# Performance work log

Hardware: AMD Instinct MI355X
Metric: run time of the kernel (lower is better)

Reference implementation:

```python
import jax, jax.numpy as jnp
import numpy as np

C = 0.01          # Poincare ball curvature 1/100
SQRT_C = 0.1
EPS = 1e-15
BALL_EPS = 4e-3   # geoopt float32 projx boundary epsilon


def _norm(x):
    return jnp.linalg.norm(x, axis=-1, keepdims=True)


def expmap0(u):
    n = jnp.maximum(_norm(u), EPS)
    return jnp.tanh(SQRT_C * n) * u / (SQRT_C * n)


def logmap0(x):
    n = jnp.maximum(_norm(x), EPS)
    t = jnp.clip(SQRT_C * n, -1.0 + 1e-7, 1.0 - 1e-7)
    return jnp.arctanh(t) * x / (SQRT_C * n)


def projx(x):
    maxnorm = (1.0 - BALL_EPS) / SQRT_C
    n = jnp.maximum(_norm(x), EPS)
    return jnp.where(n > maxnorm, x / n * maxnorm, x)


def mobius_matvec(M, x):
    xn = jnp.maximum(_norm(x), EPS)
    mx = x @ M.T
    mxn = jnp.maximum(_norm(mx), EPS)
    t = jnp.clip(SQRT_C * xn, -1.0 + 1e-7, 1.0 - 1e-7)
    res = jnp.tanh(mxn / xn * jnp.arctanh(t)) * mx / (mxn * SQRT_C)
    return jnp.where(jnp.all(mx == 0, axis=-1, keepdims=True), 0.0, res)


def mobius_add(x, y):
    x2 = jnp.sum(x * x, -1, keepdims=True)
    y2 = jnp.sum(y * y, -1, keepdims=True)
    xy = jnp.sum(x * y, -1, keepdims=True)
    num = (1 + 2 * C * xy + C * y2) * x + (1 - C * x2) * y
    den = 1 + 2 * C * xy + C * C * x2 * y2
    return num / jnp.maximum(den, EPS)


def hyp_linear(x, W, b):
    # eval mode: weight dropout is a no-op
    res = projx(mobius_matvec(W, x))
    hb = projx(expmap0(b.reshape(1, -1)))
    return projx(mobius_add(res, hb))


def setup_inputs() -> dict:
    key = jax.random.key(0)
    ks = jax.random.split(key, 10)
    B, S, N, H, HEADS, E = 2, 4, 10000, 64, 4, 160000
    G = B * S
    OC = H // HEADS
    # edges guaranteed to have no self-loops (module removes then re-adds them)
    src = jax.random.randint(ks[0], (G, E), 0, N)
    off = jax.random.randint(ks[1], (G, E), 1, N)
    dst = (src + off) % N
    edge_index = jnp.stack([src, dst], axis=1).astype(jnp.int32)  # [G,2,E]

    def glorot(k, shape, fan):
        a = np.sqrt(6.0 / fan)
        return jax.random.uniform(k, shape, minval=-a, maxval=a, dtype=jnp.float32)

    emb = jax.random.normal(ks[2], (N, H), dtype=jnp.float32)
    att_i = glorot(ks[3], (1, HEADS, OC), HEADS * OC + 1)
    att_j = glorot(ks[4], (1, HEADS, OC), HEADS * OC + 1)
    w1 = glorot(ks[5], (H, OC), H + OC)   # HypLinear(in=16, out=64): weight [out,in]
    b1 = jnp.zeros((H,), jnp.float32)
    w2 = glorot(ks[6], (H, H), H + H)
    b2 = jnp.zeros((H,), jnp.float32)
    history_graphs = jnp.zeros((B, S, N), jnp.float32)  # only shape is used
    return {"history_graphs": history_graphs, "edge_index": edge_index,
            "emb": emb, "att_i": att_i, "att_j": att_j,
            "w1": w1, "b1": b1, "w2": w2, "b2": b2}


def reference(history_graphs, edge_index, emb, att_i, att_j, w1, b1, w2, b2):
    B, S, N = history_graphs.shape
    G = edge_index.shape[0]
    H = emb.shape[1]
    heads = att_i.shape[1]
    oc = H // heads

    # node ids are arange(N) for every (b,s) -> identical features per graph
    x0 = projx(expmap0(emb))   # initHyperX, [N,H]
    xt = logmap0(x0)           # tangent features used by attention, [N,H]

    # add self loops (inputs contain none)
    loops = jnp.broadcast_to(jnp.arange(N, dtype=edge_index.dtype)[None, None, :], (G, 2, N))
    ei = jnp.concatenate([edge_index, loops], axis=-1)  # [G,2,E+N]

    def agg(e):
        src, dst = e[0], e[1]                       # targets (i), sources (j)
        x_i = xt[src].reshape(-1, heads, oc)        # [E2,h,oc]
        x_j = xt[dst].reshape(-1, heads, oc)
        alpha = jnp.sum(x_i * att_i, -1) + jnp.sum(x_j * att_j, -1)  # [E2,h]
        alpha = jax.nn.leaky_relu(alpha, 0.2)
        m = jax.ops.segment_max(alpha, src, num_segments=N)
        a = jnp.exp(alpha - m[src])
        s = jax.ops.segment_sum(a, src, num_segments=N)
        a = a / (s[src] + 1e-16)                    # edge softmax; dropout eval no-op
        sup = jax.ops.segment_sum(x_j * a[..., None], src, num_segments=N)  # [N,h,oc]
        sup = sup.mean(axis=1)                      # concat=False -> head mean, [N,oc]
        return projx(expmap0(sup))

    h = jax.vmap(agg)(ei)                           # [G,N,oc]
    node_emb = h.reshape(B, S, N, oc)[:, -1]        # last timestep, [B,N,oc]

    z = hyp_linear(node_emb, w1, b1)                # 16 -> 64
    z = projx(expmap0(jax.nn.silu(logmap0(z))))     # HypAct(SiLU)
    z = projx(expmap0(logmap0(z)))                  # HypDropout (eval: log/exp round trip)
    z = hyp_linear(z, w2, b2)                       # 64 -> 64
    return z
```

## Files before the change

kernel.cpp:

```cpp
#include <hip/hip_runtime.h>
#include <hip/hip_bf16.h>

#define N_NODES 10000
#define NE 160000
#define CAP 96
#define SQRT_C 0.1f
#define CC 0.01f
#define EPS 1e-15f
#define MAXNORM ((1.0f - 4e-3f) / SQRT_C)

__device__ __forceinline__ float fexp(float x) { return __expf(x); }
__device__ __forceinline__ float ftanh_pos(float x) {
    return 1.0f - 2.0f / (__expf(2.0f * x) + 1.0f);
}
__device__ __forceinline__ float fatanh01(float t) {
    return 0.5f * __logf((1.0f + t) / (1.0f - t));
}

__device__ __forceinline__ float ldf(const void* p, int i, int isbf) {
    return isbf ? __bfloat162float(((const __hip_bfloat16*)p)[i])
                : ((const float*)p)[i];
}

__device__ __forceinline__ int sniff_wave(const void* emb, int tid) {
    unsigned wv = ((const unsigned*)emb)[tid & 63];
    unsigned ex = (wv >> 7) & 0xFFu;
    unsigned long long m = __ballot(ex >= 116u && ex <= 133u);
    return (__popcll(m) >= 32) ? 1 : 0;
}

__device__ __forceinline__ float wsum(float v) {
#pragma unroll
    for (int off = 32; off > 0; off >>= 1) v += __shfl_xor(v, off, 64);
    return v;
}
__device__ __forceinline__ float wmax(float v) {
#pragma unroll
    for (int off = 32; off > 0; off >>= 1) v = fmaxf(v, __shfl_xor(v, off, 64));
    return v;
}

__global__ __launch_bounds__(256) void pre_scatter(const void* __restrict__ emb,
                                                   const void* __restrict__ att_i,
                                                   const void* __restrict__ att_j,
                                                   const void* __restrict__ w1g,
                                                   const void* __restrict__ b1g,
                                                   const void* __restrict__ w2g,
                                                   const void* __restrict__ b2g,
                                                   const int* __restrict__ ei,
                                                   float* __restrict__ xt,
                                                   float* __restrict__ ai,
                                                   float* __restrict__ aj,
                                                   int* __restrict__ cnt,
                                                   unsigned short* __restrict__ bucket,
                                                   int* __restrict__ ovf_cnt,
                                                   unsigned* __restrict__ ovf,
                                                   int* __restrict__ flag,
                                                   float* __restrict__ wf1t,
                                                   float* __restrict__ wf2t,
                                                   float* __restrict__ hb1f,
                                                   float* __restrict__ hb2f,
                                                   float* __restrict__ hbn2) {
    __shared__ int sflag;
    int tid = threadIdx.x;
    int w = tid >> 6, lane = tid & 63;
    if (blockIdx.x < 2500) {
        if (tid < 64) { int s = sniff_wave(emb, tid); if (tid == 0) sflag = s; }
        __syncthreads();
        int isbf = sflag;
        int t = blockIdx.x * 256 + tid;
        int node = t >> 6;
        float u = ldf(emb, node * 64 + lane, isbf);
        float n = fmaxf(sqrtf(wsum(u * u)), EPS);
        float th = ftanh_pos(SQRT_C * n);
        float x0 = th / (SQRT_C * n) * u;
        float x0n = th / SQRT_C;
        if (x0n > MAXNORM) { x0 *= MAXNORM / x0n; x0n = MAXNORM; }
        float tc = fminf(SQRT_C * x0n, 1.0f - 1e-7f);
        float xv = fatanh01(tc) / (SQRT_C * x0n) * x0;
        xt[node * 64 + lane] = xv;
        float pi = xv * ldf(att_i, lane, isbf);
        float pj = xv * ldf(att_j, lane, isbf);
#pragma unroll
        for (int off = 8; off > 0; off >>= 1) {
            pi += __shfl_xor(pi, off, 64);
            pj += __shfl_xor(pj, off, 64);
        }
        if ((lane & 15) == 0) {
            ai[node * 4 + (lane >> 4)] = pi;
            aj[node * 4 + (lane >> 4)] = pj;
        }
    } else if (blockIdx.x < 2813) {
        int e0 = (blockIdx.x - 2500) * 512 + tid;
#pragma unroll
        for (int q = 0; q < 2; ++q) {
            int e = e0 + q * 256;
            if (e >= NE) break;
            int s0 = ei[3 * 2 * NE + e], d0 = ei[3 * 2 * NE + NE + e];
            int s1 = ei[7 * 2 * NE + e], d1 = ei[7 * 2 * NE + NE + e];
            int i0 = s0, i1 = N_NODES + s1;
            int p0 = atomicAdd(&cnt[i0], 1);
            int p1 = atomicAdd(&cnt[i1], 1);
            if (p0 < CAP) bucket[i0 * CAP + p0] = (unsigned short)d0;
            else {
                int oi = atomicAdd(ovf_cnt, 1);
                ovf[oi] = (0u << 28) | ((unsigned)s0 << 14) | (unsigned)d0;
            }
            if (p1 < CAP) bucket[i1 * CAP + p1] = (unsigned short)d1;
            else {
                int oi = atomicAdd(ovf_cnt, 1);
                ovf[oi] = (1u << 28) | ((unsigned)s1 << 14) | (unsigned)d1;
            }
        }
    } else {
        if (tid < 64) { int s = sniff_wave(emb, tid); if (tid == 0) sflag = s; }
        __syncthreads();
        int isbf = sflag;
        if (tid == 0) *flag = isbf;
        for (int i = tid; i < 1024; i += 256) {
            int o = i >> 4, c = i & 15;
            wf1t[c * 64 + o] = ldf(w1g, i, isbf);
        }
        for (int i = tid; i < 4096; i += 256) {
            int o = i >> 6, c = i & 63;
            wf2t[c * 64 + o] = ldf(w2g, i, isbf);
        }
        if (w < 2) {
            const void* bg = w ? b2g : b1g;
            float b = ldf(bg, lane, isbf);
            float n = fmaxf(sqrtf(wsum(b * b)), EPS);
            float th = ftanh_pos(SQRT_C * n);
            float hv = th / (SQRT_C * n) * b;
            float hn = th / SQRT_C;
            if (hn > MAXNORM) { hv *= MAXNORM / hn; hn = MAXNORM; }
            (w ? hb2f : hb1f)[lane] = hv;
            if (lane == 0) hbn2[w] = hn * hn;
        }
    }
}

__global__ __launch_bounds__(256) void node_agg(const int* __restrict__ cnt,
                                                const unsigned short* __restrict__ bucket,
                                                const int* __restrict__ ovf_cnt,
                                                const unsigned* __restrict__ ovf,
                                                const float* __restrict__ ai,
                                                const float* __restrict__ aj,
                                                const float* __restrict__ xt,
                                                float* __restrict__ sup_t) {
    __shared__ float wlds[4][64 * 4];
    __shared__ int dlds[4][64];
    int w = threadIdx.x >> 6, lane = threadIdx.x & 63;
    int idx = blockIdx.x * 4 + w;
    int slot = (idx >= N_NODES) ? 1 : 0;
    int n = idx - slot * N_NODES;
    int deg = cnt[idx];
    int start = idx * CAP;

    float4 ai4 = *(const float4*)&ai[n * 4];
    float4 aj4n = *(const float4*)&aj[n * 4];
    float ain[4] = {ai4.x, ai4.y, ai4.z, ai4.w};
    float ajn[4] = {aj4n.x, aj4n.y, aj4n.z, aj4n.w};
    int hh = lane >> 4;
    float acc;

    if (deg <= 63) {
        bool act = (lane <= deg);
        int d = (lane < deg) ? (int)bucket[start + lane] : n;
        float4 a4 = act ? *(const float4*)&aj[d * 4] : make_float4(0.f, 0.f, 0.f, 0.f);
        float ajv[4] = {a4.x, a4.y, a4.z, a4.w};
        float eh[4];
#pragma unroll
        for (int h = 0; h < 4; ++h) {
            float a = ain[h] + ajv[h];
            a = (a < 0.0f) ? 0.2f * a : a;
            eh[h] = act ? fexp(a) : 0.0f;
        }
        float sh[4];
#pragma unroll
        for (int h = 0; h < 4; ++h) sh[h] = wsum(eh[h]);
#pragma unroll
        for (int h = 0; h < 4; ++h)
            wlds[w][lane * 4 + h] = eh[h] * (0.25f / (sh[h] + 1e-16f));
        dlds[w][lane] = d;
        int m = deg + 1;
        float s0 = 0.f, s1 = 0.f, s2 = 0.f, s3 = 0.f;
        float s4 = 0.f, s5 = 0.f, s6 = 0.f, s7 = 0.f;
        int e = 0;
        for (; e + 8 <= m; e += 8) {
            int d0 = dlds[w][e],     d1 = dlds[w][e + 1];
            int d2 = dlds[w][e + 2], d3 = dlds[w][e + 3];
            int d4 = dlds[w][e + 4], d5 = dlds[w][e + 5];
            int d6 = dlds[w][e + 6], d7 = dlds[w][e + 7];
            float w0 = wlds[w][(e + 0) * 4 + hh], w1 = wlds[w][(e + 1) * 4 + hh];
            float w2 = wlds[w][(e + 2) * 4 + hh], w3 = wlds[w][(e + 3) * 4 + hh];
            float w4 = wlds[w][(e + 4) * 4 + hh], w5 = wlds[w][(e + 5) * 4 + hh];
            float w6 = wlds[w][(e + 6) * 4 + hh], w7 = wlds[w][(e + 7) * 4 + hh];
            s0 = fmaf(w0, xt[d0 * 64 + lane], s0);
            s1 = fmaf(w1, xt[d1 * 64 + lane], s1);
            s2 = fmaf(w2, xt[d2 * 64 + lane], s2);
            s3 = fmaf(w3, xt[d3 * 64 + lane], s3);
            s4 = fmaf(w4, xt[d4 * 64 + lane], s4);
            s5 = fmaf(w5, xt[d5 * 64 + lane], s5);
            s6 = fmaf(w6, xt[d6 * 64 + lane], s6);
            s7 = fmaf(w7, xt[d7 * 64 + lane], s7);
        }
        for (; e + 4 <= m; e += 4) {
            int d0 = dlds[w][e],     d1 = dlds[w][e + 1];
            int d2 = dlds[w][e + 2], d3 = dlds[w][e + 3];
            float w0 = wlds[w][(e + 0) * 4 + hh], w1 = wlds[w][(e + 1) * 4 + hh];
            float w2 = wlds[w][(e + 2) * 4 + hh], w3 = wlds[w][(e + 3) * 4 + hh];
            s0 = fmaf(w0, xt[d0 * 64 + lane], s0);
            s1 = fmaf(w1, xt[d1 * 64 + lane], s1);
            s2 = fmaf(w2, xt[d2 * 64 + lane], s2);
            s3 = fmaf(w3, xt[d3 * 64 + lane], s3);
        }
        for (; e < m; ++e)
            s0 = fmaf(wlds[w][e * 4 + hh], xt[dlds[w][e] * 64 + lane], s0);
        acc = ((s0 + s1) + (s2 + s3)) + ((s4 + s5) + (s6 + s7));
    } else {
        int bdeg = (deg < CAP) ? deg : CAP;
        int tov = (deg > CAP) ? *ovf_cnt : 0;
        float mh[4];
#pragma unroll
        for (int h = 0; h < 4; ++h) {
            float a = ain[h] + ajn[h];
            mh[h] = (a < 0.0f) ? 0.2f * a : a;
        }
        for (int e = lane; e < bdeg; e += 64) {
            int d = bucket[start + e];
#pragma unroll
            for (int h = 0; h < 4; ++h) {
                float a = ain[h] + aj[d * 4 + h];
                a = (a < 0.0f) ? 0.2f * a : a;
                mh[h] = fmaxf(mh[h], a);
            }
        }
        for (int k = lane; k < tov; k += 64) {
            unsigned pe = ovf[k];
            if ((int)(pe >> 28) == slot && (int)((pe >> 14) & 0x3FFFu) == n) {
                int d = pe & 0x3FFFu;
#pragma unroll
                for (int h = 0; h < 4; ++h) {
                    float a = ain[h] + aj[d * 4 + h];
                    a = (a < 0.0f) ? 0.2f * a : a;
                    mh[h] = fmaxf(mh[h], a);
                }
            }
        }
#pragma unroll
        for (int h = 0; h < 4; ++h) mh[h] = wmax(mh[h]);
        float sh[4] = {0.f, 0.f, 0.f, 0.f};
        if (lane == 0) {
#pragma unroll
            for (int h = 0; h < 4; ++h) {
                float a = ain[h] + ajn[h];
                a = (a < 0.0f) ? 0.2f * a : a;
                sh[h] = fexp(a - mh[h]);
            }
        }
        for (int e = lane; e < bdeg; e += 64) {
            int d = bucket[start + e];
#pragma unroll
            for (int h = 0; h < 4; ++h) {
                float a = ain[h] + aj[d * 4 + h];
                a = (a < 0.0f) ? 0.2f * a : a;
                sh[h] += fexp(a - mh[h]);
            }
        }
        for (int k = lane; k < tov; k += 64) {
            unsigned pe = ovf[k];
            if ((int)(pe >> 28) == slot && (int)((pe >> 14) & 0x3FFFu) == n) {
                int d = pe & 0x3FFFu;
#pragma unroll
                for (int h = 0; h < 4; ++h) {
                    float a = ain[h] + aj[d * 4 + h];
                    a = (a < 0.0f) ? 0.2f * a : a;
                    sh[h] += fexp(a - mh[h]);
                }
            }
        }
#pragma unroll
        for (int h = 0; h < 4; ++h) sh[h] = wsum(sh[h]);
        float scale[4];
#pragma unroll
        for (int h = 0; h < 4; ++h) scale[h] = 0.25f / (sh[h] + 1e-16f);
        float aih = ain[hh], mhh = mh[hh], sch = scale[hh];
        float aself = aih + ajn[hh];
        aself = (aself < 0.0f) ? 0.2f * aself : aself;
        acc = fexp(aself - mhh) * sch * xt[n * 64 + lane];
        for (int e = 0; e < bdeg; ++e) {
            int d = bucket[start + e];
            float a = aih + aj[d * 4 + hh];
            a = (a < 0.0f) ? 0.2f * a : a;
            acc = fmaf(fexp(a - mhh) * sch, xt[d * 64 + lane], acc);
        }
        for (int k = 0; k < tov; ++k) {
            unsigned pe = ovf[k];
            if ((int)(pe >> 28) == slot && (int)((pe >> 14) & 0x3FFFu) == n) {
                int d = pe & 0x3FFFu;
                float a = aih + aj[d * 4 + hh];
                a = (a < 0.0f) ? 0.2f * a : a;
                acc = fmaf(fexp(a - mhh) * sch, xt[d * 64 + lane], acc);
            }
        }
    }
    acc += __shfl_xor(acc, 16, 64);
    acc += __shfl_xor(acc, 32, 64);
    if (lane < 16) sup_t[idx * 16 + lane] = acc;
}

__global__ __launch_bounds__(256) void final_stage(const float* __restrict__ sup_t,
                                                   const float* __restrict__ wf1t,
                                                   const float* __restrict__ wf2t,
                                                   const float* __restrict__ hb1f,
                                                   const float* __restrict__ hb2f,
                                                   const float* __restrict__ hbn2,
                                                   const int* __restrict__ flag,
                                                   void* __restrict__ outv) {
    __shared__ float w2s[64][68];
    int tid = threadIdx.x, w = tid >> 6, lane = tid & 63;
    for (int i = tid; i < 4096; i += 256) {
        int c = i >> 6, o = i & 63;
        w2s[o][c] = wf2t[i];
    }
    float w1r[16];
#pragma unroll
    for (int c = 0; c < 16; ++c) w1r[c] = wf1t[c * 64 + lane];
    float hb1 = hb1f[lane], hb2v = hb2f[lane];
    float y2a = hbn2[0], y2b = hbn2[1];
    int isbf = *flag;
    __syncthreads();

#pragma unroll 1
    for (int k = 0; k < 4; ++k) {
        int nd = blockIdx.x * 4 + w + k * 5000;
        float vl = (lane < 16) ? sup_t[nd * 16 + lane] : 0.0f;
        float n2 = wsum(vl * vl);
        float n = fmaxf(sqrtf(n2), EPS);
        float th0 = ftanh_pos(SQRT_C * n);
        float s0 = th0 / (SQRT_C * n);
        float x0n = th0 / SQRT_C;
        if (x0n > MAXNORM) { s0 *= MAXNORM / x0n; x0n = MAXNORM; }

        float a1 = 0.f;
#pragma unroll
        for (int c = 0; c < 16; ++c)
            a1 = fmaf(w1r[c], __shfl(vl, c, 64), a1);
        a1 *= s0;

        float mxn2 = wsum(a1 * a1);
        float mxhb = wsum(a1 * hb1);
        float xn = fmaxf(x0n, EPS);
        float mxn = fmaxf(sqrtf(mxn2), EPS);
        float t = fminf(SQRT_C * xn, 1.0f - 1e-7f);
        float th = ftanh_pos(mxn / xn * fatanh01(t));
        float rs = th / (mxn * SQRT_C);
        float rn = th / SQRT_C;
        if (mxn2 == 0.0f) { rs = 0.f; rn = 0.f; }
        if (rn > MAXNORM) { rs *= MAXNORM / rn; rn = MAXNORM; }
        float xy = rs * mxhb;
        float x2 = rn * rn;
        float A = 1.0f + 2.0f * CC * xy + CC * y2a;
        float B = 1.0f - CC * x2;
        float rden = 1.0f / fmaxf(1.0f + 2.0f * CC * xy + CC * CC * x2 * y2a, EPS);
        float z = (A * rs * a1 + B * hb1) * rden;

        float zn2 = wsum(z * z);
        float zn = fmaxf(sqrtf(zn2), EPS);
        float sc = (zn > MAXNORM) ? MAXNORM / zn : 1.0f;
        float z1n = fminf(zn, MAXNORM);
        float lg = fatanh01(fminf(SQRT_C * z1n, 1.0f - 1e-7f)) / (SQRT_C * z1n) * sc;
        float u = lg * z;
        u = u / (1.0f + __expf(-u));
        float un2 = wsum(u * u);
        float un = fmaxf(sqrtf(un2), EPS);
        float th2 = ftanh_pos(SQRT_C * un);
        float s2 = th2 / (SQRT_C * un);
        float z2n = th2 / SQRT_C;
        if (z2n > MAXNORM) { s2 *= MAXNORM / z2n; z2n = MAXNORM; }
        float z2 = u * s2;

        float a2 = 0.f;
#pragma unroll
        for (int j = 0; j < 16; ++j) {
            const float4 wq = *(const float4*)&w2s[lane][j * 4];
            a2 = fmaf(wq.x, __shfl(z2, 4 * j + 0, 64), a2);
            a2 = fmaf(wq.y, __shfl(z2, 4 * j + 1, 64), a2);
            a2 = fmaf(wq.z, __shfl(z2, 4 * j + 2, 64), a2);
            a2 = fmaf(wq.w, __shfl(z2, 4 * j + 3, 64), a2);
        }

        float pn2 = wsum(a2 * a2);
        float ph2 = wsum(a2 * hb2v);
        float xnb = fmaxf(z2n, EPS);
        float mxnb = fmaxf(sqrtf(pn2), EPS);
        float tb = fminf(SQRT_C * xnb, 1.0f - 1e-7f);
        float thb = ftanh_pos(mxnb / xnb * fatanh01(tb));
        float rsb = thb / (mxnb * SQRT_C);
        float rnb = thb / SQRT_C;
        if (pn2 == 0.0f) { rsb = 0.f; rnb = 0.f; }
        if (rnb > MAXNORM) { rsb *= MAXNORM / rnb; rnb = MAXNORM; }
        float xyb = rsb * ph2;
        float x2b = rnb * rnb;
        float Ab = 1.0f + 2.0f * CC * xyb + CC * y2b;
        float Bb = 1.0f - CC * x2b;
        float rdenb = 1.0f / fmaxf(1.0f + 2.0f * CC * xyb + CC * CC * x2b * y2b, EPS);
        float zf = (Ab * rsb * a2 + Bb * hb2v) * rdenb;
        float zf2 = wsum(zf * zf);
        float znf = fmaxf(sqrtf(zf2), EPS);
        float s4 = (znf > MAXNORM) ? MAXNORM / znf : 1.0f;
        float val = zf * s4;

        if (isbf) ((__hip_bfloat16*)outv)[nd * 64 + lane] = __float2bfloat16(val);
        else      ((float*)outv)[nd * 64 + lane] = val;
    }
}

extern "C" void kernel_launch(void* const* d_in, const int* in_sizes, int n_in,
                              void* d_out, int out_size, void* d_ws, size_t ws_size,
                              hipStream_t stream) {
    const int* ei = (const int*)d_in[1];
    const void* emb   = d_in[2];
    const void* att_i = d_in[3];
    const void* att_j = d_in[4];
    const void* w1 = d_in[5];
    const void* b1 = d_in[6];
    const void* w2 = d_in[7];
    const void* b2 = d_in[8];

    float* ws = (float*)d_ws;
    float* xt    = ws;
    float* ai    = ws + 640000;
    float* aj    = ws + 680000;
    float* sup_t = ws + 720000;
    int* cnt     = (int*)(ws + 1040000);
    int* ovf_cnt = (int*)(ws + 1060000);
    unsigned short* bucket = (unsigned short*)(ws + 1060032);
    unsigned* ovf = (unsigned*)(ws + 2020032);
    int* flag     = (int*)(ws + 2340032);
    float* wf1t = ws + 2340064;
    float* wf2t = ws + 2341088;
    float* hb1f = ws + 2345184;
    float* hb2f = ws + 2345248;
    float* hbn2 = ws + 2345312;

    hipMemsetAsync((void*)cnt, 0, (2 * N_NODES + 8) * sizeof(int), stream);
    hipLaunchKernelGGL(pre_scatter, dim3(2814), dim3(256), 0, stream,
                       emb, att_i, att_j, w1, b1, w2, b2, ei,
                       xt, ai, aj, cnt, bucket, ovf_cnt, ovf, flag,
                       wf1t, wf2t, hb1f, hb2f, hbn2);
    hipLaunchKernelGGL(node_agg, dim3(5000), dim3(256), 0, stream,
                       cnt, bucket, ovf_cnt, ovf, ai, aj, xt, sup_t);
    hipLaunchKernelGGL(final_stage, dim3(1250), dim3(256), 0, stream,
                       sup_t, wf1t, wf2t, hb1f, hb2f, hbn2, flag, d_out);
}
```

Before: 161.4 us.

## Rework final stage: DPP reductions, register-resident W2, LDS-broadcast matvecs

Replaces the butterfly shuffle reductions in final_stage with a DPP row-shift/row-broadcast reduction followed by a readlane. W2 now lives in registers per lane instead of a transposed LDS tile, which drops the block-wide __syncthreads. The matvec inputs are broadcast through a small per-wave LDS buffer instead of per-element __shfl. Each wave now handles four consecutive nodes, with their inputs prefetched up front. The extra 64 registers per lane may lower occupancy, and the DPP masks have to be correct for wave64.

```diff
diff --git a/kernel.cpp b/kernel.cpp
--- a/kernel.cpp
+++ b/kernel.cpp
@@ -38,6 +38,23 @@
 #pragma unroll
     for (int off = 32; off > 0; off >>= 1) v = fmaxf(v, __shfl_xor(v, off, 64));
     return v;
+}
+
+__device__ __forceinline__ float dpp_wsum(float x) {
+    int t;
+    t = __builtin_amdgcn_update_dpp(0, __float_as_int(x), 0x111, 0xF, 0xF, true);
+    x += __int_as_float(t);
+    t = __builtin_amdgcn_update_dpp(0, __float_as_int(x), 0x112, 0xF, 0xF, true);
+    x += __int_as_float(t);
+    t = __builtin_amdgcn_update_dpp(0, __float_as_int(x), 0x114, 0xF, 0xE, true);
+    x += __int_as_float(t);
+    t = __builtin_amdgcn_update_dpp(0, __float_as_int(x), 0x118, 0xF, 0xC, true);
+    x += __int_as_float(t);
+    t = __builtin_amdgcn_update_dpp(0, __float_as_int(x), 0x142, 0xA, 0xF, true);
+    x += __int_as_float(t);
+    t = __builtin_amdgcn_update_dpp(0, __float_as_int(x), 0x143, 0xC, 0xF, true);
+    x += __int_as_float(t);
+    return __int_as_float(__builtin_amdgcn_readlane(__float_as_int(x), 63));
 }
 
 __global__ __launch_bounds__(256) void pre_scatter(const void* __restrict__ emb,
@@ -317,25 +334,31 @@
                                                    const float* __restrict__ hbn2,
                                                    const int* __restrict__ flag,
                                                    void* __restrict__ outv) {
-    __shared__ float w2s[64][68];
+    __shared__ float vz[4][80];
     int tid = threadIdx.x, w = tid >> 6, lane = tid & 63;
-    for (int i = tid; i < 4096; i += 256) {
-        int c = i >> 6, o = i & 63;
-        w2s[o][c] = wf2t[i];
-    }
+    float w2r[64];
+#pragma unroll
+    for (int c = 0; c < 64; ++c) w2r[c] = wf2t[c * 64 + lane];
     float w1r[16];
 #pragma unroll
     for (int c = 0; c < 16; ++c) w1r[c] = wf1t[c * 64 + lane];
     float hb1 = hb1f[lane], hb2v = hb2f[lane];
     float y2a = hbn2[0], y2b = hbn2[1];
     int isbf = *flag;
-    __syncthreads();
+    float* vbuf = vz[w];
+    float* zbuf = vz[w] + 16;
+    int nb = (blockIdx.x * 4 + w) * 4;
+
+    float vls[4];
+#pragma unroll
+    for (int k = 0; k < 4; ++k)
+        vls[k] = (lane < 16) ? sup_t[(nb + k) * 16 + lane] : 0.0f;
 
 #pragma unroll 1
     for (int k = 0; k < 4; ++k) {
-        int nd = blockIdx.x * 4 + w + k * 5000;
-        float vl = (lane < 16) ? sup_t[nd * 16 + lane] : 0.0f;
-        float n2 = wsum(vl * vl);
+        float vl = vls[k];
+        if (lane < 16) vbuf[lane] = vl;
+        float n2 = dpp_wsum(vl * vl);
         float n = fmaxf(sqrtf(n2), EPS);
         float th0 = ftanh_pos(SQRT_C * n);
         float s0 = th0 / (SQRT_C * n);
@@ -344,12 +367,17 @@
 
         float a1 = 0.f;
 #pragma unroll
-        for (int c = 0; c < 16; ++c)
-            a1 = fmaf(w1r[c], __shfl(vl, c, 64), a1);
+        for (int j = 0; j < 4; ++j) {
+            const float4 vq = *(const float4*)&vbuf[j * 4];
+            a1 = fmaf(w1r[4 * j + 0], vq.x, a1);
+            a1 = fmaf(w1r[4 * j + 1], vq.y, a1);
+            a1 = fmaf(w1r[4 * j + 2], vq.z, a1);
+            a1 = fmaf(w1r[4 * j + 3], vq.w, a1);
+        }
         a1 *= s0;
 
-        float mxn2 = wsum(a1 * a1);
-        float mxhb = wsum(a1 * hb1);
+        float mxn2 = dpp_wsum(a1 * a1);
+        float mxhb = dpp_wsum(a1 * hb1);
         float xn = fmaxf(x0n, EPS);
         float mxn = fmaxf(sqrtf(mxn2), EPS);
         float t = fminf(SQRT_C * xn, 1.0f - 1e-7f);
@@ -365,14 +393,15 @@
         float rden = 1.0f / fmaxf(1.0f + 2.0f * CC * xy + CC * CC * x2 * y2a, EPS);
         float z = (A * rs * a1 + B * hb1) * rden;
 
-        float zn2 = wsum(z * z);
+        float zn2 = dpp_wsum(z * z);
         float zn = fmaxf(sqrtf(zn2), EPS);
         float sc = (zn > MAXNORM) ? MAXNORM / zn : 1.0f;
         float z1n = fminf(zn, MAXNORM);
         float lg = fatanh01(fminf(SQRT_C * z1n, 1.0f - 1e-7f)) / (SQRT_C * z1n) * sc;
         float u = lg * z;
         u = u / (1.0f + __expf(-u));
-        float un2 = wsum(u * u);
+
+        float un2 = dpp_wsum(u * u);
         float un = fmaxf(sqrtf(un2), EPS);
         float th2 = ftanh_pos(SQRT_C * un);
         float s2 = th2 / (SQRT_C * un);
@@ -380,18 +409,19 @@
         if (z2n > MAXNORM) { s2 *= MAXNORM / z2n; z2n = MAXNORM; }
         float z2 = u * s2;
 
+        zbuf[lane] = z2;
         float a2 = 0.f;
 #pragma unroll
         for (int j = 0; j < 16; ++j) {
-            const float4 wq = *(const float4*)&w2s[lane][j * 4];
-            a2 = fmaf(wq.x, __shfl(z2, 4 * j + 0, 64), a2);
-            a2 = fmaf(wq.y, __shfl(z2, 4 * j + 1, 64), a2);
-            a2 = fmaf(wq.z, __shfl(z2, 4 * j + 2, 64), a2);
-            a2 = fmaf(wq.w, __shfl(z2, 4 * j + 3, 64), a2);
-        }
-
-        float pn2 = wsum(a2 * a2);
-        float ph2 = wsum(a2 * hb2v);
+            const float4 zq = *(const float4*)&zbuf[j * 4];
+            a2 = fmaf(w2r[4 * j + 0], zq.x, a2);
+            a2 = fmaf(w2r[4 * j + 1], zq.y, a2);
+            a2 = fmaf(w2r[4 * j + 2], zq.z, a2);
+            a2 = fmaf(w2r[4 * j + 3], zq.w, a2);
+        }
+
+        float pn2 = dpp_wsum(a2 * a2);
+        float ph2 = dpp_wsum(a2 * hb2v);
         float xnb = fmaxf(z2n, EPS);
         float mxnb = fmaxf(sqrtf(pn2), EPS);
         float tb = fminf(SQRT_C * xnb, 1.0f - 1e-7f);
@@ -406,13 +436,13 @@
         float Bb = 1.0f - CC * x2b;
         float rdenb = 1.0f / fmaxf(1.0f + 2.0f * CC * xyb + CC * CC * x2b * y2b, EPS);
         float zf = (Ab * rsb * a2 + Bb * hb2v) * rdenb;
-        float zf2 = wsum(zf * zf);
+        float zf2 = dpp_wsum(zf * zf);
         float znf = fmaxf(sqrtf(zf2), EPS);
         float s4 = (znf > MAXNORM) ? MAXNORM / znf : 1.0f;
         float val = zf * s4;
 
-        if (isbf) ((__hip_bfloat16*)outv)[nd * 64 + lane] = __float2bfloat16(val);
-        else      ((float*)outv)[nd * 64 + lane] = val;
+        if (isbf) ((__hip_bfloat16*)outv)[(nb + k) * 64 + lane] = __float2bfloat16(val);
+        else      ((float*)outv)[(nb + k) * 64 + lane] = val;
     }
 }
 
```

Result: faster. 144.8 us (-10.3%).
